# Kernel optimization log

Measured on AMD Instinct MI355X. Metric: run time of the kernel, lower is better.

## Reference

```python
import jax, jax.numpy as jnp
import numpy as np

COMMITMENT_COST = 0.25


def setup_inputs() -> dict:
    key = jax.random.key(0)
    k1, k2 = jax.random.split(key)
    x = jax.random.normal(k1, (4, 64, 32, 32, 32), dtype=jnp.float32)
    weight = jax.random.normal(k2, (512, 64), dtype=jnp.float32)
    return {"x": x, "weight": weight}


def reference(x, weight):
    b, c, h, w, d = x.shape  # c == embed_dim
    # [b, h, w, d, c] -> [N, c]
    flat = jnp.transpose(x, (0, 2, 3, 4, 1)).reshape(-1, c)
    # squared L2 distances to each codebook vector: [N, n_embed]
    distances = (
        jnp.sum(flat * flat, axis=1, keepdims=True)
        - 2.0 * (flat @ weight.T)
        + jnp.sum(weight * weight, axis=1)
    )
    embed_idx_flat = jnp.argmin(distances, axis=1)  # == argmax(-distances)
    embed_idx = embed_idx_flat.reshape(b, h, w, d)
    # gather codebook rows and move embed dim back to channel position
    quantized = jnp.transpose(weight[embed_idx], (0, 4, 1, 2, 3))  # [b, c, h, w, d]
    latent_loss = COMMITMENT_COST * jnp.mean(
        (jax.lax.stop_gradient(quantized) - x) ** 2
    )
    quantized_st = jax.lax.stop_gradient(quantized - x) + x
    return quantized_st, embed_idx, latent_loss
```

## Files before the change

kernel.cpp:

```cpp
#include <hip/hip_runtime.h>
#include <hip/hip_bf16.h>

#define HWD      32768
#define NC       64
#define NE       512
#define OUT_IDX  8388608
#define OUT_LOSS 8519680

#define WS_WSQ_F   16
#define WS_WP_B    4096
#define WS_NEEDED  200704

typedef __attribute__((ext_vector_type(8))) short bf16x8;
typedef __attribute__((ext_vector_type(4))) float f32x4;

__device__ inline unsigned short bf16_rne(float v) {
    unsigned u = __builtin_bit_cast(unsigned, v);
    return (unsigned short)((u + 0x7FFFu + ((u >> 16) & 1u)) >> 16);
}
__device__ inline float bf16_f(unsigned short s) {
    return __builtin_bit_cast(float, (unsigned)s << 16);
}
__device__ inline void split3(float v, unsigned short& h, unsigned short& m,
                              unsigned short& l) {
    h = bf16_rne(v);
    float r1 = v - bf16_f(h);
    m = bf16_rne(r1);
    float r2 = r1 - bf16_f(m);
    l = bf16_rne(r2);
}

__global__ __launch_bounds__(256) void vq_prep(
    const float* __restrict__ w, float* __restrict__ ws)
{
    const int gtid = blockIdx.x * 256 + threadIdx.x;
    if (gtid == 0) { ws[0] = 0.f; ((unsigned*)ws)[1] = 0u; }
    if (gtid < NE) {
        const float4* row = (const float4*)(w + (size_t)gtid * NC);
        float s0 = 0.f, s1 = 0.f, s2 = 0.f, s3 = 0.f;
#pragma unroll
        for (int k = 0; k < 16; ++k) {
            float4 v = row[k];
            s0 = fmaf(v.x, v.x, s0); s1 = fmaf(v.y, v.y, s1);
            s2 = fmaf(v.z, v.z, s2); s3 = fmaf(v.w, v.w, s3);
        }
        ws[WS_WSQ_F + gtid] = (s0 + s1) + (s2 + s3);
    }
    const int lane_s = gtid & 63;
    int t = gtid >> 6;
    const int plane = t % 3; t /= 3;
    const int kc = t & 1;
    const int ct = t >> 1;
    const int code = ct * 16 + (lane_s & 15);
    const int kb   = kc * 32 + (lane_s >> 4) * 8;
    const float* src = w + (size_t)code * NC + kb;
    unsigned short o[8];
#pragma unroll
    for (int j = 0; j < 8; ++j) {
        unsigned short h, m, l;
        split3(src[j], h, m, l);
        o[j] = (plane == 0) ? h : (plane == 1) ? m : l;
    }
    unsigned short* dst = (unsigned short*)((char*)ws + WS_WP_B) + (size_t)gtid * 8;
#pragma unroll
    for (int j = 0; j < 8; ++j) dst[j] = o[j];
}

__global__ __launch_bounds__(256, 4) void vq_fused2(
    const float* __restrict__ x, const float* __restrict__ w,
    float* __restrict__ ws, float* __restrict__ out)
{
    __shared__ float q_sh[128 * 65];
    __shared__ int   idx_sh[128];
    __shared__ float wred[4];

    const int tid    = threadIdx.x;
    const int wv     = tid >> 6;
    const int lane   = tid & 63;
    const int lanelo = lane & 15;
    const int quad   = lane >> 4;
    const int posB   = blockIdx.x * 128;
    const int b      = posB >> 15;
    const int hwdB   = posB & (HWD - 1);
    const size_t xoff = (size_t)b * NC * HWD + hwdB;
    const int wpos   = wv * 32;

    bf16x8 A[2][2][3];
    float  xsqp[2];
#pragma unroll
    for (int pt = 0; pt < 2; ++pt) {
        float xs = 0.f;
#pragma unroll
        for (int kc = 0; kc < 2; ++kc) {
            bf16x8 fh, fm, fl;
#pragma unroll
            for (int j = 0; j < 8; ++j) {
                const int k = kc * 32 + quad * 8 + j;
                const float v = x[xoff + (size_t)k * HWD + wpos + pt * 16 + lanelo];
                unsigned short h, m, l;
                split3(v, h, m, l);
                fh[j] = (short)h; fm[j] = (short)m; fl[j] = (short)l;
                xs = fmaf(v, v, xs);
            }
            A[pt][kc][0] = fh; A[pt][kc][1] = fm; A[pt][kc][2] = fl;
        }
        xs += __shfl_xor(xs, 16);
        xs += __shfl_xor(xs, 32);
        xsqp[pt] = xs;
    }
    float xsq_r[2][4];
#pragma unroll
    for (int pt = 0; pt < 2; ++pt)
#pragma unroll
        for (int r = 0; r < 4; ++r)
            xsq_r[pt][r] = __shfl(xsqp[pt], quad * 4 + r);

    const bf16x8* wp   = (const bf16x8*)((const char*)ws + WS_WP_B);
    const float*  wsqp = ws + WS_WSQ_F;

    float best[2][4];
    int   bidx[2][4];
#pragma unroll
    for (int pt = 0; pt < 2; ++pt)
#pragma unroll
        for (int r = 0; r < 4; ++r) { best[pt][r] = 3.402823466e38f; bidx[pt][r] = 0; }

    for (int ct = 0; ct < 32; ++ct) {
        bf16x8 B[2][3];
#pragma unroll
        for (int kc = 0; kc < 2; ++kc)
#pragma unroll
            for (int p = 0; p < 3; ++p)
                B[kc][p] = wp[(size_t)((ct * 2 + kc) * 3 + p) * 64 + lane];
        const float wsq_c = wsqp[ct * 16 + lanelo];

#pragma unroll
        for (int pt = 0; pt < 2; ++pt) {
            f32x4 acc = {0.f, 0.f, 0.f, 0.f};
            acc = __builtin_amdgcn_mfma_f32_16x16x32_bf16(A[pt][0][2], B[0][0], acc, 0, 0, 0);
            acc = __builtin_amdgcn_mfma_f32_16x16x32_bf16(A[pt][1][2], B[1][0], acc, 0, 0, 0);
            acc = __builtin_amdgcn_mfma_f32_16x16x32_bf16(A[pt][0][1], B[0][1], acc, 0, 0, 0);
            acc = __builtin_amdgcn_mfma_f32_16x16x32_bf16(A[pt][1][1], B[1][1], acc, 0, 0, 0);
            acc = __builtin_amdgcn_mfma_f32_16x16x32_bf16(A[pt][0][0], B[0][2], acc, 0, 0, 0);
            acc = __builtin_amdgcn_mfma_f32_16x16x32_bf16(A[pt][1][0], B[1][2], acc, 0, 0, 0);
            acc = __builtin_amdgcn_mfma_f32_16x16x32_bf16(A[pt][0][1], B[0][0], acc, 0, 0, 0);
            acc = __builtin_amdgcn_mfma_f32_16x16x32_bf16(A[pt][1][1], B[1][0], acc, 0, 0, 0);
            acc = __builtin_amdgcn_mfma_f32_16x16x32_bf16(A[pt][0][0], B[0][1], acc, 0, 0, 0);
            acc = __builtin_amdgcn_mfma_f32_16x16x32_bf16(A[pt][1][0], B[1][1], acc, 0, 0, 0);
            acc = __builtin_amdgcn_mfma_f32_16x16x32_bf16(A[pt][0][0], B[0][0], acc, 0, 0, 0);
            acc = __builtin_amdgcn_mfma_f32_16x16x32_bf16(A[pt][1][0], B[1][0], acc, 0, 0, 0);
#pragma unroll
            for (int r = 0; r < 4; ++r) {
                const float d = fmaf(-2.f, acc[r], xsq_r[pt][r]) + wsq_c;
                const int ge = ct * 16 + lanelo;
                if (d < best[pt][r]) { best[pt][r] = d; bidx[pt][r] = ge; }
            }
        }
    }

#pragma unroll
    for (int pt = 0; pt < 2; ++pt)
#pragma unroll
        for (int r = 0; r < 4; ++r) {
            float d = best[pt][r]; int i = bidx[pt][r];
#pragma unroll
            for (int mlane = 1; mlane <= 8; mlane <<= 1) {
                const float d2 = __shfl_xor(d, mlane);
                const int   i2 = __shfl_xor(i, mlane);
                if (d2 < d || (d2 == d && i2 < i)) { d = d2; i = i2; }
            }
            if (lanelo == 0)
                idx_sh[wpos + pt * 16 + quad * 4 + r] = i;
        }
    __syncthreads();

    if (tid < 128) out[OUT_IDX + posB + tid] = (float)idx_sh[tid];

#pragma unroll
    for (int it = 0; it < 32; ++it) {
        const int e = it * 256 + tid;
        const int r = e >> 6, c = e & 63;
        q_sh[r * 65 + c] = w[(size_t)idx_sh[r] * NC + c];
    }
    __syncthreads();

    float lsum = 0.f;
#pragma unroll
    for (int it = 0; it < 32; ++it) {
        const int e = it * 256 + tid;
        const int c = e >> 7;
        const int p = e & 127;
        const size_t off = xoff + (size_t)c * HWD + p;
        const float xv = x[off];
        const float q  = q_sh[p * 65 + c];
        const float dq = q - xv;
        lsum = fmaf(dq, dq, lsum);
        out[off] = dq + xv;
    }

#pragma unroll
    for (int off = 32; off >= 1; off >>= 1) lsum += __shfl_down(lsum, off);
    if (lane == 0) wred[wv] = lsum;
    __syncthreads();
    if (tid == 0) {
        atomicAdd((float*)ws, (wred[0] + wred[1]) + (wred[2] + wred[3]));
        __threadfence();
        const unsigned done = atomicAdd((unsigned*)ws + 1, 1u);
        if (done == 1023u) {
            const float L = atomicAdd((float*)ws, 0.f);
            out[OUT_LOSS] = 0.25f * L / 8388608.0f;
        }
    }
}

__global__ __launch_bounds__(256, 2) void vq_fused_fb(
    const float* __restrict__ x, const float* __restrict__ w,
    float* __restrict__ out, float* __restrict__ loss_acc)
{
    __shared__ float lw[256 * NC];
    __shared__ float wsq[256];
    __shared__ float wred[4];
    const int tid = threadIdx.x;
    const int n0  = blockIdx.x * 512;
    const int b   = n0 >> 15;
    const int hwd = (n0 & (HWD - 1)) + tid;
    const float* xp = x + (size_t)b * NC * HWD + hwd;
    float xr0[NC], xr1[NC];
#pragma unroll
    for (int c = 0; c < NC; ++c) { xr0[c] = xp[(size_t)c * HWD]; xr1[c] = xp[(size_t)c * HWD + 256]; }
    float xsq0 = 0.f, xsq1 = 0.f;
#pragma unroll
    for (int c = 0; c < NC; ++c) { xsq0 = fmaf(xr0[c], xr0[c], xsq0); xsq1 = fmaf(xr1[c], xr1[c], xsq1); }
    float best0 = 3.402823466e38f, best1 = 3.402823466e38f;
    int bi0 = 0, bi1 = 0;
    for (int pass = 0; pass < 2; ++pass) {
        if (pass) __syncthreads();
        const float4* wt = (const float4*)(w + pass * 256 * NC);
        float4* l4 = (float4*)lw;
#pragma unroll
        for (int k = 0; k < 16; ++k) l4[tid + k * 256] = wt[tid + k * 256];
        {
            const float4* row = wt + tid * 16;
            float s0 = 0.f, s1 = 0.f, s2 = 0.f, s3 = 0.f;
#pragma unroll
            for (int k = 0; k < 16; ++k) {
                float4 v = row[k];
                s0 = fmaf(v.x, v.x, s0); s1 = fmaf(v.y, v.y, s1);
                s2 = fmaf(v.z, v.z, s2); s3 = fmaf(v.w, v.w, s3);
            }
            wsq[tid] = (s0 + s1) + (s2 + s3);
        }
        __syncthreads();
#pragma unroll 2
        for (int e = 0; e < 256; ++e) {
            const float4* row = (const float4*)(lw + e * NC);
            float a0 = 0.f, a1 = 0.f, c0 = 0.f, c1 = 0.f;
#pragma unroll
            for (int k = 0; k < 16; ++k) {
                float4 v = row[k];
                a0 = fmaf(xr0[4 * k + 0], v.x, a0); a1 = fmaf(xr0[4 * k + 1], v.y, a1);
                a0 = fmaf(xr0[4 * k + 2], v.z, a0); a1 = fmaf(xr0[4 * k + 3], v.w, a1);
                c0 = fmaf(xr1[4 * k + 0], v.x, c0); c1 = fmaf(xr1[4 * k + 1], v.y, c1);
                c0 = fmaf(xr1[4 * k + 2], v.z, c0); c1 = fmaf(xr1[4 * k + 3], v.w, c1);
            }
            const float d0 = (xsq0 - 2.f * (a0 + a1)) + wsq[e];
            const float d1 = (xsq1 - 2.f * (c0 + c1)) + wsq[e];
            const int ge = pass * 256 + e;
            if (d0 < best0) { best0 = d0; bi0 = ge; }
            if (d1 < best1) { best1 = d1; bi1 = ge; }
        }
    }
    float* o0 = out + (size_t)b * NC * HWD + hwd;
    float lsum = 0.f;
    const float4* r0 = (const float4*)(w + bi0 * NC);
    const float4* r1 = (const float4*)(w + bi1 * NC);
#pragma unroll
    for (int k = 0; k < 16; ++k) {
        float4 q0 = r0[k], q1 = r1[k];
        float qv0[4] = { q0.x, q0.y, q0.z, q0.w };
        float qv1[4] = { q1.x, q1.y, q1.z, q1.w };
#pragma unroll
        for (int j = 0; j < 4; ++j) {
            const int c = 4 * k + j;
            const float dv0 = qv0[j] - xr0[c];
            const float dv1 = qv1[j] - xr1[c];
            lsum = fmaf(dv0, dv0, lsum); lsum = fmaf(dv1, dv1, lsum);
            o0[(size_t)c * HWD] = dv0 + xr0[c];
            o0[(size_t)c * HWD + 256] = dv1 + xr1[c];
        }
    }
    const int n = b * HWD + hwd;
    out[OUT_IDX + n] = (float)bi0;
    out[OUT_IDX + n + 256] = (float)bi1;
#pragma unroll
    for (int off = 32; off >= 1; off >>= 1) lsum += __shfl_down(lsum, off);
    if ((tid & 63) == 0) wred[tid >> 6] = lsum;
    __syncthreads();
    if (tid == 0) atomicAdd(loss_acc, (wred[0] + wred[1]) + (wred[2] + wred[3]));
}

__global__ void vq_loss_fin_fb(const float* __restrict__ acc, float* __restrict__ out)
{
    out[OUT_LOSS] = 0.25f * acc[0] / 8388608.0f;
}

extern "C" void kernel_launch(void* const* d_in, const int* in_sizes, int n_in,
                              void* d_out, int out_size, void* d_ws, size_t ws_size,
                              hipStream_t stream)
{
    const float* x = (const float*)d_in[0];
    const float* w = (const float*)d_in[1];
    float* out = (float*)d_out;
    float* ws  = (float*)d_ws;

    if (ws_size >= WS_NEEDED) {
        vq_prep<<<48, 256, 0, stream>>>(w, ws);
        vq_fused2<<<1024, 256, 0, stream>>>(x, w, ws, out);
    } else {
        hipMemsetAsync(d_ws, 0, sizeof(float), stream);
        vq_fused_fb<<<256, 256, 0, stream>>>(x, w, out, ws);
        vq_loss_fin_fb<<<1, 1, 0, stream>>>(ws, out);
    }
}
```

Before: 167.0 us.

## Stage codebook split planes through LDS in chunks shared by the block

Instead of each wave reading the pre-split bf16 codebook planes from global memory, the block cooperatively copies 48KB stages of the codebook into shared memory (four stages) and the waves read B fragments from LDS. The squared codebook norms are also cached in LDS, and the LDS buffer is reused for the quantized gather. Occupancy bound drops from 4 to 3 blocks per CU because of the larger LDS footprint. The copy is not overlapped with compute, so it adds syncs and exposed load phases in exchange for fewer redundant global/L2 reads.

```diff
diff --git a/kernel.cpp b/kernel.cpp
--- a/kernel.cpp
+++ b/kernel.cpp
@@ -10,6 +10,7 @@
 #define WS_WSQ_F   16
 #define WS_WP_B    4096
 #define WS_NEEDED  200704
+#define STAGE_B    49152
 
 typedef __attribute__((ext_vector_type(8))) short bf16x8;
 typedef __attribute__((ext_vector_type(4))) float f32x4;
@@ -66,11 +67,12 @@
     for (int j = 0; j < 8; ++j) dst[j] = o[j];
 }
 
-__global__ __launch_bounds__(256, 4) void vq_fused2(
+__global__ __launch_bounds__(256, 3) void vq_fused2(
     const float* __restrict__ x, const float* __restrict__ w,
     float* __restrict__ ws, float* __restrict__ out)
 {
-    __shared__ float q_sh[128 * 65];
+    __shared__ __align__(16) unsigned char smem[STAGE_B];
+    __shared__ float wsq_lds[NE];
     __shared__ int   idx_sh[128];
     __shared__ float wred[4];
 
@@ -85,6 +87,19 @@
     const size_t xoff = (size_t)b * NC * HWD + hwdB;
     const int wpos   = wv * 32;
 
+    auto copy_stage = [&](int s) {
+        const float4* src = (const float4*)((const char*)ws + WS_WP_B
+                                            + (size_t)s * STAGE_B);
+        float4* dst = (float4*)smem;
+#pragma unroll
+        for (int it = 0; it < 12; ++it)
+            dst[it * 256 + tid] = src[it * 256 + tid];
+    };
+
+    copy_stage(0);
+    wsq_lds[tid]       = ws[WS_WSQ_F + tid];
+    wsq_lds[256 + tid] = ws[WS_WSQ_F + 256 + tid];
+
     bf16x8 A[2][2][3];
     float  xsqp[2];
 #pragma unroll
@@ -115,9 +130,6 @@
         for (int r = 0; r < 4; ++r)
             xsq_r[pt][r] = __shfl(xsqp[pt], quad * 4 + r);
 
-    const bf16x8* wp   = (const bf16x8*)((const char*)ws + WS_WP_B);
-    const float*  wsqp = ws + WS_WSQ_F;
-
     float best[2][4];
     int   bidx[2][4];
 #pragma unroll
@@ -125,36 +137,48 @@
 #pragma unroll
         for (int r = 0; r < 4; ++r) { best[pt][r] = 3.402823466e38f; bidx[pt][r] = 0; }
 
-    for (int ct = 0; ct < 32; ++ct) {
-        bf16x8 B[2][3];
-#pragma unroll
-        for (int kc = 0; kc < 2; ++kc)
-#pragma unroll
-            for (int p = 0; p < 3; ++p)
-                B[kc][p] = wp[(size_t)((ct * 2 + kc) * 3 + p) * 64 + lane];
-        const float wsq_c = wsqp[ct * 16 + lanelo];
-
-#pragma unroll
-        for (int pt = 0; pt < 2; ++pt) {
-            f32x4 acc = {0.f, 0.f, 0.f, 0.f};
-            acc = __builtin_amdgcn_mfma_f32_16x16x32_bf16(A[pt][0][2], B[0][0], acc, 0, 0, 0);
-            acc = __builtin_amdgcn_mfma_f32_16x16x32_bf16(A[pt][1][2], B[1][0], acc, 0, 0, 0);
-            acc = __builtin_amdgcn_mfma_f32_16x16x32_bf16(A[pt][0][1], B[0][1], acc, 0, 0, 0);
-            acc = __builtin_amdgcn_mfma_f32_16x16x32_bf16(A[pt][1][1], B[1][1], acc, 0, 0, 0);
-            acc = __builtin_amdgcn_mfma_f32_16x16x32_bf16(A[pt][0][0], B[0][2], acc, 0, 0, 0);
-            acc = __builtin_amdgcn_mfma_f32_16x16x32_bf16(A[pt][1][0], B[1][2], acc, 0, 0, 0);
-            acc = __builtin_amdgcn_mfma_f32_16x16x32_bf16(A[pt][0][1], B[0][0], acc, 0, 0, 0);
-            acc = __builtin_amdgcn_mfma_f32_16x16x32_bf16(A[pt][1][1], B[1][0], acc, 0, 0, 0);
-            acc = __builtin_amdgcn_mfma_f32_16x16x32_bf16(A[pt][0][0], B[0][1], acc, 0, 0, 0);
-            acc = __builtin_amdgcn_mfma_f32_16x16x32_bf16(A[pt][1][0], B[1][1], acc, 0, 0, 0);
-            acc = __builtin_amdgcn_mfma_f32_16x16x32_bf16(A[pt][0][0], B[0][0], acc, 0, 0, 0);
-            acc = __builtin_amdgcn_mfma_f32_16x16x32_bf16(A[pt][1][0], B[1][0], acc, 0, 0, 0);
-#pragma unroll
-            for (int r = 0; r < 4; ++r) {
-                const float d = fmaf(-2.f, acc[r], xsq_r[pt][r]) + wsq_c;
-                const int ge = ct * 16 + lanelo;
-                if (d < best[pt][r]) { best[pt][r] = d; bidx[pt][r] = ge; }
-            }
+    const bf16x8* lb = (const bf16x8*)smem;
+
+#pragma unroll 1
+    for (int s = 0; s < 4; ++s) {
+        __syncthreads();
+#pragma unroll
+        for (int ctl = 0; ctl < 8; ++ctl) {
+            const int ct = s * 8 + ctl;
+            bf16x8 B[2][3];
+#pragma unroll
+            for (int kc = 0; kc < 2; ++kc)
+#pragma unroll
+                for (int p = 0; p < 3; ++p)
+                    B[kc][p] = lb[(size_t)((ctl * 2 + kc) * 3 + p) * 64 + lane];
+            const float wsq_c = wsq_lds[ct * 16 + lanelo];
+
+#pragma unroll
+            for (int pt = 0; pt < 2; ++pt) {
+                f32x4 acc = {0.f, 0.f, 0.f, 0.f};
+                acc = __builtin_amdgcn_mfma_f32_16x16x32_bf16(A[pt][0][2], B[0][0], acc, 0, 0, 0);
+                acc = __builtin_amdgcn_mfma_f32_16x16x32_bf16(A[pt][1][2], B[1][0], acc, 0, 0, 0);
+                acc = __builtin_amdgcn_mfma_f32_16x16x32_bf16(A[pt][0][1], B[0][1], acc, 0, 0, 0);
+                acc = __builtin_amdgcn_mfma_f32_16x16x32_bf16(A[pt][1][1], B[1][1], acc, 0, 0, 0);
+                acc = __builtin_amdgcn_mfma_f32_16x16x32_bf16(A[pt][0][0], B[0][2], acc, 0, 0, 0);
+                acc = __builtin_amdgcn_mfma_f32_16x16x32_bf16(A[pt][1][0], B[1][2], acc, 0, 0, 0);
+                acc = __builtin_amdgcn_mfma_f32_16x16x32_bf16(A[pt][0][1], B[0][0], acc, 0, 0, 0);
+                acc = __builtin_amdgcn_mfma_f32_16x16x32_bf16(A[pt][1][1], B[1][0], acc, 0, 0, 0);
+                acc = __builtin_amdgcn_mfma_f32_16x16x32_bf16(A[pt][0][0], B[0][1], acc, 0, 0, 0);
+                acc = __builtin_amdgcn_mfma_f32_16x16x32_bf16(A[pt][1][0], B[1][1], acc, 0, 0, 0);
+                acc = __builtin_amdgcn_mfma_f32_16x16x32_bf16(A[pt][0][0], B[0][0], acc, 0, 0, 0);
+                acc = __builtin_amdgcn_mfma_f32_16x16x32_bf16(A[pt][1][0], B[1][0], acc, 0, 0, 0);
+#pragma unroll
+                for (int r = 0; r < 4; ++r) {
+                    const float d = fmaf(-2.f, acc[r], xsq_r[pt][r]) + wsq_c;
+                    const int ge = ct * 16 + lanelo;
+                    if (d < best[pt][r]) { best[pt][r] = d; bidx[pt][r] = ge; }
+                }
+            }
+        }
+        if (s < 3) {
+            __syncthreads();
+            copy_stage(s + 1);
         }
     }
 
@@ -176,6 +200,7 @@
 
     if (tid < 128) out[OUT_IDX + posB + tid] = (float)idx_sh[tid];
 
+    float* q_sh = (float*)smem;
 #pragma unroll
     for (int it = 0; it < 32; ++it) {
         const int e = it * 256 + tid;
```

Result: slower. 186.0 us (+11.4%).
